# Kernel optimization log

Hardware: AMD Instinct MI355X
Metric: run time of the kernel (lower is better)

## Reference

```python
import jax, jax.numpy as jnp
import numpy as np
from functools import partial

N_NODES = 50000
N_EDGES = 800000
EMBED_DIM = 128
NUM_GROUPS = 3
T = 1.0


def setup_inputs() -> dict:
    key = jax.random.key(0)
    k1, k2, k3, k4 = jax.random.split(key, 4)
    node_feature = jax.random.normal(k1, (N_NODES, EMBED_DIM), dtype=jnp.float32)
    src = jax.random.randint(k2, (N_EDGES,), 0, N_NODES, dtype=jnp.int32)
    dst = jax.random.randint(k3, (N_EDGES,), 0, N_NODES, dtype=jnp.int32)
    W = jax.random.normal(k4, (EMBED_DIM, NUM_GROUPS), dtype=jnp.float32) / np.sqrt(EMBED_DIM)
    b = jnp.zeros((NUM_GROUPS,), dtype=jnp.float32)
    return {"node_feature": node_feature, "src": src, "dst": dst, "W": W, "b": b}


def reference(node_feature, src, dst, W, b):
    n = node_feature.shape[0]
    # linear + softmax group scores: [N, G]
    coeff = jax.nn.softmax((node_feature @ W + b) / T, axis=1)
    # weighted individual features: [N, G, D]
    wif = node_feature[:, None, :] * coeff[:, :, None]
    # message: gather src features per edge; reduce: mean over in-neighbors
    summed = jax.ops.segment_sum(wif[src], dst, num_segments=n)  # [N, G, D]
    deg = jax.ops.segment_sum(jnp.ones_like(dst, dtype=node_feature.dtype), dst, num_segments=n)
    group_feat = summed / jnp.maximum(deg, 1.0)[:, None, None]  # mean; zero-degree -> 0
    # weighted sum over groups with destination's own incidence coeff: [N, D]
    weighted_group_feat = jnp.einsum('ngd,ng->nd', group_feat, coeff)
    return weighted_group_feat
```

## Files before the change

kernel.cpp:

```cpp
#include <hip/hip_runtime.h>
#include <hip/hip_bf16.h>

#define D 128
#define G 3
#define BN 128
#define CH 8192
#define BIN_T 1024
#define CAP 4096
#define REG 8192

__device__ __forceinline__ float b2f(unsigned short u) {
    return __uint_as_float((unsigned int)u << 16);
}

__global__ __launch_bounds__(256) void lg_coeff_kernel(
        const float* __restrict__ X, const float* __restrict__ W,
        const float* __restrict__ b, float4* __restrict__ coeff,
        __hip_bfloat16* __restrict__ Xh,
        int* __restrict__ cursor, int nbuck,
        int n) {
    if (cursor && blockIdx.x == 0) {
        for (int i = threadIdx.x; i < nbuck; i += 256) cursor[i] = 0;
    }
    int node = (int)((blockIdx.x * (size_t)blockDim.x + threadIdx.x) >> 6);
    int lane = threadIdx.x & 63;
    if (node >= n) return;
    float2 x = ((const float2*)(X + (size_t)node * D))[lane];
    if (Xh) {
        __hip_bfloat162 h2;
        h2.x = __float2bfloat16(x.x);
        h2.y = __float2bfloat16(x.y);
        ((__hip_bfloat162*)(Xh + (size_t)node * D))[lane] = h2;
    }
    int d0 = lane * 2;
    float s0 = x.x * W[d0 * G + 0] + x.y * W[(d0 + 1) * G + 0];
    float s1 = x.x * W[d0 * G + 1] + x.y * W[(d0 + 1) * G + 1];
    float s2 = x.x * W[d0 * G + 2] + x.y * W[(d0 + 1) * G + 2];
    #pragma unroll
    for (int off = 32; off; off >>= 1) {
        s0 += __shfl_xor(s0, off);
        s1 += __shfl_xor(s1, off);
        s2 += __shfl_xor(s2, off);
    }
    s0 += b[0]; s1 += b[1]; s2 += b[2];
    float m = fmaxf(s0, fmaxf(s1, s2));
    float e0 = __expf(s0 - m), e1 = __expf(s1 - m), e2 = __expf(s2 - m);
    float inv = 1.0f / (e0 + e1 + e2);
    if (lane == 0) coeff[node] = make_float4(e0 * inv, e1 * inv, e2 * inv, 0.0f);
}

__global__ __launch_bounds__(BIN_T) void lg_bin_kernel(
        const int* __restrict__ src, const int* __restrict__ dst,
        int* __restrict__ cursor, unsigned int* __restrict__ temp,
        int E, int nbuck) {
    __shared__ unsigned int stage[CH];
    __shared__ unsigned short stage_bk[CH];
    __shared__ int hist[512], hbase[512], hcnt[512], gbs[512];
    int tid = threadIdx.x;
    int wv = tid >> 6, ln = tid & 63;
    int e0 = blockIdx.x * CH;
    int ecnt = min(CH, E - e0);
    for (int i = tid; i < 512; i += BIN_T) { hist[i] = 0; hcnt[i] = 0; }
    __syncthreads();
    int rs[CH / BIN_T], rd[CH / BIN_T];
    #pragma unroll
    for (int u = 0; u < CH / BIN_T; ++u) {
        int k = tid + u * BIN_T;
        if (k < ecnt) {
            rs[u] = src[e0 + k];
            rd[u] = dst[e0 + k];
            atomicAdd(&hist[rd[u] >> 7], 1);
        } else rd[u] = -1;
    }
    __syncthreads();
    if (wv == 0) {
        int c[8]; int tot = 0;
        #pragma unroll
        for (int t = 0; t < 8; ++t) { c[t] = hist[ln * 8 + t]; tot += c[t]; }
        int s = tot;
        #pragma unroll
        for (int o = 1; o < 64; o <<= 1) {
            int y = __shfl_up(s, o);
            if (ln >= o) s += y;
        }
        int run = s - tot;
        #pragma unroll
        for (int t = 0; t < 8; ++t) { hbase[ln * 8 + t] = run; run += c[t]; }
    }
    __syncthreads();
    #pragma unroll
    for (int u = 0; u < CH / BIN_T; ++u) {
        if (rd[u] >= 0) {
            int bk = rd[u] >> 7;
            int idx = hbase[bk] + atomicAdd(&hcnt[bk], 1);
            stage[idx] = ((unsigned int)rs[u] & 0xFFFFu) |
                         (((unsigned int)rd[u] & 127u) << 16);
            stage_bk[idx] = (unsigned short)bk;
        }
    }
    for (int i = tid; i < nbuck; i += BIN_T) {
        int c = hist[i];
        gbs[i] = c ? atomicAdd(&cursor[i], c) : 0;
    }
    __syncthreads();
    for (int k = tid; k < ecnt; k += BIN_T) {
        int bk = stage_bk[k];
        int pos = gbs[bk] + (k - hbase[bk]);
        if (pos < REG) temp[(size_t)bk * REG + pos] = stage[k];
    }
}

__global__ __launch_bounds__(1024) void lg_sortagg_kernel(
        const __hip_bfloat16* __restrict__ Xh,
        const float4* __restrict__ coeff,
        const unsigned int* __restrict__ temp,
        const int* __restrict__ cursor,
        float* __restrict__ out, int n) {
    __shared__ unsigned int stage[CAP];
    __shared__ float4 cdl[BN];
    __shared__ int nhist[BN], nbase[BN], ncur[BN];
    int tid = threadIdx.x;
    int wv = tid >> 6, ln = tid & 63;
    int nb0 = blockIdx.x * BN;
    int nv = min(BN, n - nb0);
    const unsigned int* rg = temp + (size_t)blockIdx.x * REG;
    int count = min(cursor[blockIdx.x], REG);
    if (tid < BN) { nhist[tid] = 0; ncur[tid] = 0; }
    if (tid < nv) cdl[tid] = coeff[nb0 + tid];
    __syncthreads();

    if (count <= CAP) {
        int base = tid * 4;
        unsigned int r0 = 0, r1 = 0, r2 = 0, r3 = 0;
        if (base + 3 < count) {
            uint4 R = *(const uint4*)(rg + base);
            r0 = R.x; r1 = R.y; r2 = R.z; r3 = R.w;
            atomicAdd(&nhist[(r0 >> 16) & 127u], 1);
            atomicAdd(&nhist[(r1 >> 16) & 127u], 1);
            atomicAdd(&nhist[(r2 >> 16) & 127u], 1);
            atomicAdd(&nhist[(r3 >> 16) & 127u], 1);
        } else {
            if (base + 0 < count) { r0 = rg[base + 0]; atomicAdd(&nhist[(r0 >> 16) & 127u], 1); }
            if (base + 1 < count) { r1 = rg[base + 1]; atomicAdd(&nhist[(r1 >> 16) & 127u], 1); }
            if (base + 2 < count) { r2 = rg[base + 2]; atomicAdd(&nhist[(r2 >> 16) & 127u], 1); }
            if (base + 3 < count) { r3 = rg[base + 3]; atomicAdd(&nhist[(r3 >> 16) & 127u], 1); }
        }
        __syncthreads();
        if (wv == 0) {
            int a = nhist[2 * ln], b2 = nhist[2 * ln + 1];
            int tot = a + b2;
            int s = tot;
            #pragma unroll
            for (int o = 1; o < 64; o <<= 1) {
                int y = __shfl_up(s, o);
                if (ln >= o) s += y;
            }
            int excl = s - tot;
            nbase[2 * ln] = excl;
            nbase[2 * ln + 1] = excl + a;
        }
        __syncthreads();
        auto place = [&](unsigned int rec) {
            int s = (int)(rec & 0xFFFFu);
            int d = (int)((rec >> 16) & 127u);
            float4 cs = coeff[s];
            float4 cd = cdl[d];
            float w = cs.x * cd.x + cs.y * cd.y + cs.z * cd.z;
            unsigned int wb = __float_as_uint(w);
            wb += 0x7FFFu + ((wb >> 16) & 1u);
            int pos = nbase[d] + atomicAdd(&ncur[d], 1);
            stage[pos] = (rec & 0xFFFFu) | (wb & 0xFFFF0000u);
        };
        if (base + 0 < count) place(r0);
        if (base + 1 < count) place(r1);
        if (base + 2 < count) place(r2);
        if (base + 3 < count) place(r3);
        __syncthreads();
        int sub = ln & 31;
        bool hiHalf = (ln >= 32);
        for (int i = wv; i < nv; i += 16) {
            int ibeg = nbase[i];
            int icnt = nhist[i];
            float4 acc = make_float4(0.0f, 0.0f, 0.0f, 0.0f);
            int j = 0;
            for (; j + 3 < icnt; j += 4) {
                unsigned int a0 = stage[ibeg + j + 0];
                unsigned int a1 = stage[ibeg + j + 1];
                unsigned int b0 = stage[ibeg + j + 2];
                unsigned int b1 = stage[ibeg + j + 3];
                unsigned int qa = hiHalf ? a1 : a0;
                unsigned int qb = hiHalf ? b1 : b0;
                float wa = __uint_as_float(qa & 0xFFFF0000u);
                float wb = __uint_as_float(qb & 0xFFFF0000u);
                ushort4 ha = ((const ushort4*)(Xh + (size_t)(qa & 0xFFFFu) * D))[sub];
                ushort4 hb = ((const ushort4*)(Xh + (size_t)(qb & 0xFFFFu) * D))[sub];
                acc.x = fmaf(wa, b2f(ha.x), acc.x);
                acc.y = fmaf(wa, b2f(ha.y), acc.y);
                acc.z = fmaf(wa, b2f(ha.z), acc.z);
                acc.w = fmaf(wa, b2f(ha.w), acc.w);
                acc.x = fmaf(wb, b2f(hb.x), acc.x);
                acc.y = fmaf(wb, b2f(hb.y), acc.y);
                acc.z = fmaf(wb, b2f(hb.z), acc.z);
                acc.w = fmaf(wb, b2f(hb.w), acc.w);
            }
            for (; j < icnt; j += 2) {
                unsigned int a0 = stage[ibeg + j];
                unsigned int a1 = (j + 1 < icnt) ? stage[ibeg + j + 1]
                                                 : (a0 & 0xFFFFu);
                unsigned int qa = hiHalf ? a1 : a0;
                float wa = __uint_as_float(qa & 0xFFFF0000u);
                ushort4 ha = ((const ushort4*)(Xh + (size_t)(qa & 0xFFFFu) * D))[sub];
                acc.x = fmaf(wa, b2f(ha.x), acc.x);
                acc.y = fmaf(wa, b2f(ha.y), acc.y);
                acc.z = fmaf(wa, b2f(ha.z), acc.z);
                acc.w = fmaf(wa, b2f(ha.w), acc.w);
            }
            acc.x += __shfl_xor(acc.x, 32);
            acc.y += __shfl_xor(acc.y, 32);
            acc.z += __shfl_xor(acc.z, 32);
            acc.w += __shfl_xor(acc.w, 32);
            float invd = 1.0f / fmaxf((float)icnt, 1.0f);
            if (!hiHalf)
                ((float4*)(out + (size_t)(nb0 + i) * D))[sub] =
                    make_float4(acc.x * invd, acc.y * invd,
                                acc.z * invd, acc.w * invd);
        }
    } else {
        for (int k = tid; k < count; k += 1024)
            atomicAdd(&nhist[(rg[k] >> 16) & 127u], 1);
        __syncthreads();
        for (int i = wv; i < nv; i += 16) {
            float4 cd = cdl[i];
            float accx = 0.0f, accy = 0.0f;
            for (int bb = 0; bb < count; bb += 64) {
                int k = bb + ln;
                unsigned int rec = (k < count) ? rg[k] : 0u;
                bool ok = (k < count) && ((int)((rec >> 16) & 127u) == i);
                unsigned long long mask = __ballot(ok);
                while (mask) {
                    int bpos = __ffsll((long long)mask) - 1;
                    mask &= mask - 1;
                    unsigned int rr = __shfl(rec, bpos);
                    int s0 = (int)(rr & 0xFFFFu);
                    float4 cs = coeff[s0];
                    float w = cs.x * cd.x + cs.y * cd.y + cs.z * cd.z;
                    __hip_bfloat162 h0 = ((const __hip_bfloat162*)(Xh + (size_t)s0 * D))[ln];
                    accx = fmaf(w, __bfloat162float(h0.x), accx);
                    accy = fmaf(w, __bfloat162float(h0.y), accy);
                }
            }
            float invd = 1.0f / fmaxf((float)nhist[i], 1.0f);
            ((float2*)(out + (size_t)(nb0 + i) * D))[ln] =
                make_float2(accx * invd, accy * invd);
        }
    }
}

__global__ void lg_deg_kernel(const int* __restrict__ dst, int* __restrict__ deg, int E) {
    int e = (int)(blockIdx.x * (size_t)blockDim.x + threadIdx.x);
    if (e < E) atomicAdd(&deg[dst[e]], 1);
}

__global__ void lg_scatter_kernel(const float* __restrict__ X,
                                  const float4* __restrict__ coeff,
                                  const int* __restrict__ src, const int* __restrict__ dst,
                                  float* __restrict__ out, int E) {
    int e = (int)((blockIdx.x * (size_t)blockDim.x + threadIdx.x) >> 6);
    int lane = threadIdx.x & 63;
    if (e >= E) return;
    int s = src[e], d = dst[e];
    float4 cs = coeff[s], cd = coeff[d];
    float se = cs.x * cd.x + cs.y * cd.y + cs.z * cd.z;
    float2 x = ((const float2*)(X + (size_t)s * D))[lane];
    atomicAdd(&out[(size_t)d * D + lane * 2 + 0], se * x.x);
    atomicAdd(&out[(size_t)d * D + lane * 2 + 1], se * x.y);
}

__global__ void lg_scale_kernel(float* __restrict__ out, const int* __restrict__ deg, int n) {
    int node = (int)((blockIdx.x * (size_t)blockDim.x + threadIdx.x) >> 6);
    int lane = threadIdx.x & 63;
    if (node >= n) return;
    float invd = 1.0f / fmaxf((float)deg[node], 1.0f);
    float2* p = (float2*)(out + (size_t)node * D);
    float2 v = p[lane];
    p[lane] = make_float2(v.x * invd, v.y * invd);
}

extern "C" void kernel_launch(void* const* d_in, const int* in_sizes, int n_in,
                              void* d_out, int out_size, void* d_ws, size_t ws_size,
                              hipStream_t stream) {
    const float* X   = (const float*)d_in[0];
    const int*   src = (const int*)d_in[1];
    const int*   dst = (const int*)d_in[2];
    const float* W   = (const float*)d_in[3];
    const float* b   = (const float*)d_in[4];
    float* out = (float*)d_out;
    int n = in_sizes[0] / D;
    int E = in_sizes[1];

    int nbuck  = (n + BN - 1) / BN;
    int nchunk = (E + CH - 1) / CH;

    char* ws = (char*)d_ws;
    size_t p = 0;
    auto alloc = [&](size_t bytes) -> void* {
        void* r = ws + p;
        p = (p + bytes + 255) & ~(size_t)255;
        return r;
    };
    float4* coeff  = (float4*)alloc((size_t)n * sizeof(float4));
    int*    cursor = (int*)alloc((size_t)nbuck * sizeof(int));
    unsigned int* temp = (unsigned int*)alloc((size_t)nbuck * REG * sizeof(unsigned int));
    __hip_bfloat16* Xh = (__hip_bfloat16*)alloc((size_t)n * D * sizeof(__hip_bfloat16));
    size_t p_full = p;
    int*    deg    = (int*)alloc((size_t)n * sizeof(int));

    int node_blocks = (n + 3) / 4;
    int edge_blocks = (E + 255) / 256;

    bool fast_ok = (n <= 65536) && (nbuck <= 512) && (p_full <= ws_size);
    if (fast_ok) {
        lg_coeff_kernel<<<node_blocks, 256, 0, stream>>>(X, W, b, coeff, Xh,
                                                         cursor, nbuck, n);
        lg_bin_kernel<<<nchunk, BIN_T, 0, stream>>>(src, dst, cursor, temp, E, nbuck);
        lg_sortagg_kernel<<<nbuck, 1024, 0, stream>>>(Xh, coeff, temp, cursor, out, n);
    } else {
        hipMemsetAsync(deg, 0, (size_t)n * sizeof(int), stream);
        hipMemsetAsync(out, 0, (size_t)n * D * sizeof(float), stream);
        lg_coeff_kernel<<<node_blocks, 256, 0, stream>>>(X, W, b, coeff, nullptr,
                                                         nullptr, 0, n);
        lg_deg_kernel<<<edge_blocks, 256, 0, stream>>>(dst, deg, E);
        lg_scatter_kernel<<<(E + 3) / 4, 256, 0, stream>>>(X, coeff, src, dst, out, E);
        lg_scale_kernel<<<node_blocks, 256, 0, stream>>>(out, deg, n);
    }
}
```

Baseline: 62.11 us.

## Split each 128-node bucket across two 512-thread blocks and widen gather unroll

The sort-aggregate kernel now launches two blocks per bucket, each owning 64 destination nodes and filtering records by bit 22 of the packed destination. With about 391 buckets on a many-CU GPU, this roughly doubles the block count for better CU occupancy, and it halves the LDS stage buffer. The cost is that both blocks read the whole bucket region, so record traffic doubles. The gather loop is also unrolled to 8 edges per iteration (4 per half-wave) to keep more independent bf16 row loads in flight.

Result: slower. 66.08 us (+6.4%).

```diff
diff --git a/kernel.cpp b/kernel.cpp
--- a/kernel.cpp
+++ b/kernel.cpp
@@ -4,9 +4,10 @@
 #define D 128
 #define G 3
 #define BN 128
+#define HBN 64
 #define CH 8192
 #define BIN_T 1024
-#define CAP 4096
+#define HCAP 2048
 #define REG 8192
 
 __device__ __forceinline__ float b2f(unsigned short u) {
@@ -110,59 +111,63 @@
     }
 }
 
-__global__ __launch_bounds__(1024) void lg_sortagg_kernel(
+__global__ __launch_bounds__(512) void lg_sortagg_kernel(
         const __hip_bfloat16* __restrict__ Xh,
         const float4* __restrict__ coeff,
         const unsigned int* __restrict__ temp,
         const int* __restrict__ cursor,
         float* __restrict__ out, int n) {
-    __shared__ unsigned int stage[CAP];
-    __shared__ float4 cdl[BN];
-    __shared__ int nhist[BN], nbase[BN], ncur[BN];
+    __shared__ unsigned int stage[HCAP];
+    __shared__ float4 cdl[HBN];
+    __shared__ int nhist[HBN], nbase[HBN], ncur[HBN];
+    __shared__ int stot;
     int tid = threadIdx.x;
     int wv = tid >> 6, ln = tid & 63;
-    int nb0 = blockIdx.x * BN;
-    int nv = min(BN, n - nb0);
-    const unsigned int* rg = temp + (size_t)blockIdx.x * REG;
-    int count = min(cursor[blockIdx.x], REG);
-    if (tid < BN) { nhist[tid] = 0; ncur[tid] = 0; }
+    int bucket = blockIdx.x >> 1;
+    unsigned int half = blockIdx.x & 1;
+    int nb0 = bucket * BN + (int)half * HBN;
+    int nv = min(HBN, n - nb0);
+    if (nv <= 0) return;
+    const unsigned int* rg = temp + (size_t)bucket * REG;
+    int count = min(cursor[bucket], REG);
+    if (tid < HBN) { nhist[tid] = 0; ncur[tid] = 0; }
     if (tid < nv) cdl[tid] = coeff[nb0 + tid];
     __syncthreads();
 
-    if (count <= CAP) {
-        int base = tid * 4;
-        unsigned int r0 = 0, r1 = 0, r2 = 0, r3 = 0;
+    for (int base = tid * 4; base < count; base += 2048) {
         if (base + 3 < count) {
             uint4 R = *(const uint4*)(rg + base);
-            r0 = R.x; r1 = R.y; r2 = R.z; r3 = R.w;
-            atomicAdd(&nhist[(r0 >> 16) & 127u], 1);
-            atomicAdd(&nhist[(r1 >> 16) & 127u], 1);
-            atomicAdd(&nhist[(r2 >> 16) & 127u], 1);
-            atomicAdd(&nhist[(r3 >> 16) & 127u], 1);
+            if (((R.x >> 22) & 1u) == half) atomicAdd(&nhist[(R.x >> 16) & 63u], 1);
+            if (((R.y >> 22) & 1u) == half) atomicAdd(&nhist[(R.y >> 16) & 63u], 1);
+            if (((R.z >> 22) & 1u) == half) atomicAdd(&nhist[(R.z >> 16) & 63u], 1);
+            if (((R.w >> 22) & 1u) == half) atomicAdd(&nhist[(R.w >> 16) & 63u], 1);
         } else {
-            if (base + 0 < count) { r0 = rg[base + 0]; atomicAdd(&nhist[(r0 >> 16) & 127u], 1); }
-            if (base + 1 < count) { r1 = rg[base + 1]; atomicAdd(&nhist[(r1 >> 16) & 127u], 1); }
-            if (base + 2 < count) { r2 = rg[base + 2]; atomicAdd(&nhist[(r2 >> 16) & 127u], 1); }
-            if (base + 3 < count) { r3 = rg[base + 3]; atomicAdd(&nhist[(r3 >> 16) & 127u], 1); }
-        }
-        __syncthreads();
-        if (wv == 0) {
-            int a = nhist[2 * ln], b2 = nhist[2 * ln + 1];
-            int tot = a + b2;
-            int s = tot;
-            #pragma unroll
-            for (int o = 1; o < 64; o <<= 1) {
-                int y = __shfl_up(s, o);
-                if (ln >= o) s += y;
-            }
-            int excl = s - tot;
-            nbase[2 * ln] = excl;
-            nbase[2 * ln + 1] = excl + a;
-        }
-        __syncthreads();
+            for (int t = base; t < count; ++t) {
+                unsigned int r = rg[t];
+                if (((r >> 22) & 1u) == half) atomicAdd(&nhist[(r >> 16) & 63u], 1);
+            }
+        }
+    }
+    __syncthreads();
+    if (wv == 0) {
+        int a = nhist[ln];
+        int s = a;
+        #pragma unroll
+        for (int o = 1; o < 64; o <<= 1) {
+            int y = __shfl_up(s, o);
+            if (ln >= o) s += y;
+        }
+        nbase[ln] = s - a;
+        if (ln == 63) stot = s;
+    }
+    __syncthreads();
+    int mine = stot;
+
+    if (mine <= HCAP) {
         auto place = [&](unsigned int rec) {
+            if (((rec >> 22) & 1u) != half) return;
             int s = (int)(rec & 0xFFFFu);
-            int d = (int)((rec >> 16) & 127u);
+            int d = (int)((rec >> 16) & 63u);
             float4 cs = coeff[s];
             float4 cd = cdl[d];
             float w = cs.x * cd.x + cs.y * cd.y + cs.z * cd.z;
@@ -171,29 +176,35 @@
             int pos = nbase[d] + atomicAdd(&ncur[d], 1);
             stage[pos] = (rec & 0xFFFFu) | (wb & 0xFFFF0000u);
         };
-        if (base + 0 < count) place(r0);
-        if (base + 1 < count) place(r1);
-        if (base + 2 < count) place(r2);
-        if (base + 3 < count) place(r3);
+        for (int base = tid * 4; base < count; base += 2048) {
+            if (base + 3 < count) {
+                uint4 R = *(const uint4*)(rg + base);
+                place(R.x); place(R.y); place(R.z); place(R.w);
+            } else {
+                for (int t = base; t < count; ++t) place(rg[t]);
+            }
+        }
         __syncthreads();
         int sub = ln & 31;
         bool hiHalf = (ln >= 32);
-        for (int i = wv; i < nv; i += 16) {
+        for (int i = wv; i < nv; i += 8) {
             int ibeg = nbase[i];
             int icnt = nhist[i];
             float4 acc = make_float4(0.0f, 0.0f, 0.0f, 0.0f);
             int j = 0;
-            for (; j + 3 < icnt; j += 4) {
-                unsigned int a0 = stage[ibeg + j + 0];
-                unsigned int a1 = stage[ibeg + j + 1];
-                unsigned int b0 = stage[ibeg + j + 2];
-                unsigned int b1 = stage[ibeg + j + 3];
-                unsigned int qa = hiHalf ? a1 : a0;
-                unsigned int qb = hiHalf ? b1 : b0;
+            for (; j + 7 < icnt; j += 8) {
+                unsigned int qa = stage[ibeg + j + 0 + (hiHalf ? 1 : 0)];
+                unsigned int qb = stage[ibeg + j + 2 + (hiHalf ? 1 : 0)];
+                unsigned int qc = stage[ibeg + j + 4 + (hiHalf ? 1 : 0)];
+                unsigned int qd = stage[ibeg + j + 6 + (hiHalf ? 1 : 0)];
+                ushort4 ha = ((const ushort4*)(Xh + (size_t)(qa & 0xFFFFu) * D))[sub];
+                ushort4 hb = ((const ushort4*)(Xh + (size_t)(qb & 0xFFFFu) * D))[sub];
+                ushort4 hc = ((const ushort4*)(Xh + (size_t)(qc & 0xFFFFu) * D))[sub];
+                ushort4 hd = ((const ushort4*)(Xh + (size_t)(qd & 0xFFFFu) * D))[sub];
                 float wa = __uint_as_float(qa & 0xFFFF0000u);
                 float wb = __uint_as_float(qb & 0xFFFF0000u);
-                ushort4 ha = ((const ushort4*)(Xh + (size_t)(qa & 0xFFFFu) * D))[sub];
-                ushort4 hb = ((const ushort4*)(Xh + (size_t)(qb & 0xFFFFu) * D))[sub];
+                float wc = __uint_as_float(qc & 0xFFFF0000u);
+                float wd = __uint_as_float(qd & 0xFFFF0000u);
                 acc.x = fmaf(wa, b2f(ha.x), acc.x);
                 acc.y = fmaf(wa, b2f(ha.y), acc.y);
                 acc.z = fmaf(wa, b2f(ha.z), acc.z);
@@ -202,6 +213,14 @@
                 acc.y = fmaf(wb, b2f(hb.y), acc.y);
                 acc.z = fmaf(wb, b2f(hb.z), acc.z);
                 acc.w = fmaf(wb, b2f(hb.w), acc.w);
+                acc.x = fmaf(wc, b2f(hc.x), acc.x);
+                acc.y = fmaf(wc, b2f(hc.y), acc.y);
+                acc.z = fmaf(wc, b2f(hc.z), acc.z);
+                acc.w = fmaf(wc, b2f(hc.w), acc.w);
+                acc.x = fmaf(wd, b2f(hd.x), acc.x);
+                acc.y = fmaf(wd, b2f(hd.y), acc.y);
+                acc.z = fmaf(wd, b2f(hd.z), acc.z);
+                acc.w = fmaf(wd, b2f(hd.w), acc.w);
             }
             for (; j < icnt; j += 2) {
                 unsigned int a0 = stage[ibeg + j];
@@ -226,16 +245,14 @@
                                 acc.z * invd, acc.w * invd);
         }
     } else {
-        for (int k = tid; k < count; k += 1024)
-            atomicAdd(&nhist[(rg[k] >> 16) & 127u], 1);
-        __syncthreads();
-        for (int i = wv; i < nv; i += 16) {
+        for (int i = wv; i < nv; i += 8) {
             float4 cd = cdl[i];
+            unsigned int want = (half << 6) | (unsigned int)i;
             float accx = 0.0f, accy = 0.0f;
             for (int bb = 0; bb < count; bb += 64) {
                 int k = bb + ln;
                 unsigned int rec = (k < count) ? rg[k] : 0u;
-                bool ok = (k < count) && ((int)((rec >> 16) & 127u) == i);
+                bool ok = (k < count) && (((rec >> 16) & 127u) == want);
                 unsigned long long mask = __ballot(ok);
                 while (mask) {
                     int bpos = __ffsll((long long)mask) - 1;
@@ -323,7 +340,7 @@
         lg_coeff_kernel<<<node_blocks, 256, 0, stream>>>(X, W, b, coeff, Xh,
                                                          cursor, nbuck, n);
         lg_bin_kernel<<<nchunk, BIN_T, 0, stream>>>(src, dst, cursor, temp, E, nbuck);
-        lg_sortagg_kernel<<<nbuck, 1024, 0, stream>>>(Xh, coeff, temp, cursor, out, n);
+        lg_sortagg_kernel<<<2 * nbuck, 512, 0, stream>>>(Xh, coeff, temp, cursor, out, n);
     } else {
         hipMemsetAsync(deg, 0, (size_t)n * sizeof(int), stream);
         hipMemsetAsync(out, 0, (size_t)n * D * sizeof(float), stream);
```
